# Performance work log

Hardware: AMD Instinct MI355X
Metric: run time of the kernel (lower is better)

## Reference

```python
import jax, jax.numpy as jnp
import numpy as np

N_NODES = 100000
N_EDGES = 1600000
NFEAT, NHID, NCLASS = 512, 256, 128
K_HOPS = 5
ALPHA = 0.1


def setup_inputs() -> dict:
    key = jax.random.key(0)
    ks = jax.random.split(key, 7)
    x = jax.random.normal(ks[0], (N_NODES, NFEAT), dtype=jnp.float32)
    edge_index = jax.random.randint(ks[1], (2, N_EDGES), 0, N_NODES, dtype=jnp.int64)
    edge_weight = jax.random.uniform(ks[2], (N_EDGES,), dtype=jnp.float32)
    # Glorot-ish scaled linear weights
    W1 = jax.random.normal(ks[3], (NFEAT, NHID), dtype=jnp.float32) * (1.0 / np.sqrt(NFEAT))
    b1 = jnp.zeros((NHID,), dtype=jnp.float32)
    W2 = jax.random.normal(ks[4], (NHID, NCLASS), dtype=jnp.float32) * (1.0 / np.sqrt(NHID))
    b2 = jnp.zeros((NCLASS,), dtype=jnp.float32)
    return {"x": x, "edge_index": edge_index, "edge_weight": edge_weight,
            "W1": W1, "b1": b1, "W2": W2, "b2": b2}


def reference(x, edge_index, edge_weight, W1, b1, W2, b2):
    # 2-layer MLP (act after first layer only; dropout p=0)
    h = jnp.maximum(x @ W1 + b1, 0.0)
    h = h @ W2 + b2  # [N, nclass]
    src = edge_index[0]
    dst = edge_index[1]
    x0 = h

    def step(carry, _):
        # gather by source, scale by edge weight, scatter-add at target
        msg = carry[src] * edge_weight[:, None]          # [E, nclass]
        agg = jax.ops.segment_sum(msg, dst, num_segments=N_NODES)
        out = (1.0 - ALPHA) * agg + ALPHA * x0           # restart mix
        return out, None

    xK, _ = jax.lax.scan(step, x0, None, length=K_HOPS)
    return jax.nn.log_softmax(xK, axis=1)
```

## Files before the change

### kernel.cpp

```cpp
#include <hip/hip_runtime.h>
#include <hip/hip_bf16.h>
#include <cstdint>
#include <cstddef>

#define N_NODES 100000
#define NFEAT 512
#define NHID 256
#define NCLASS 128
#define K_HOPS 5
#define ALPHA 0.1f

typedef __attribute__((ext_vector_type(8))) short short8v;
typedef __attribute__((ext_vector_type(4))) float f32x4;

__device__ __forceinline__ unsigned short f2bf(float f) {
    unsigned u = __builtin_bit_cast(unsigned, f);
    u += 0x7FFFu + ((u >> 16) & 1u);
    return (unsigned short)(u >> 16);
}
__device__ __forceinline__ float bflo(unsigned u) {
    return __builtin_bit_cast(float, u << 16);
}
__device__ __forceinline__ float bfhi(unsigned u) {
    return __builtin_bit_cast(float, u & 0xFFFF0000u);
}


__global__ void count_kernel(const int* __restrict__ dst, int* __restrict__ counts, int E) {
    int i = blockIdx.x * blockDim.x + threadIdx.x;
    if (i < E) atomicAdd(&counts[dst[i]], 1);
}

__global__ __launch_bounds__(256) void scan_p1(const int* __restrict__ counts,
                                               int* __restrict__ partial, int n) {
    __shared__ int ws[4];
    int b = blockIdx.x, t = threadIdx.x;
    int base = b * 1024 + t * 4;
    int s = 0;
#pragma unroll
    for (int j = 0; j < 4; ++j) {
        int idx = base + j;
        if (idx < n) s += counts[idx];
    }
#pragma unroll
    for (int off = 32; off; off >>= 1) s += __shfl_xor(s, off, 64);
    if ((t & 63) == 0) ws[t >> 6] = s;
    __syncthreads();
    if (t == 0) partial[b] = ws[0] + ws[1] + ws[2] + ws[3];
}

__global__ __launch_bounds__(128) void scan_p2(int* __restrict__ partial, int nb) {
    __shared__ int s[128];
    int t = threadIdx.x;
    int v = (t < nb) ? partial[t] : 0;
    s[t] = v;
    __syncthreads();
    for (int off = 1; off < 128; off <<= 1) {
        int u = (t >= off) ? s[t - off] : 0;
        __syncthreads();
        s[t] += u;
        __syncthreads();
    }
    if (t < nb) partial[t] = (t == 0) ? 0 : s[t - 1];
}

__global__ __launch_bounds__(256) void scan_p3(const int* __restrict__ counts,
                                               const int* __restrict__ partial,
                                               int* __restrict__ row_ptr,
                                               int* __restrict__ fill, int n) {
    __shared__ int ts[256];
    int b = blockIdx.x, t = threadIdx.x;
    int base = b * 1024 + t * 4;
    int c[4];
#pragma unroll
    for (int j = 0; j < 4; ++j) {
        int idx = base + j;
        c[j] = (idx < n) ? counts[idx] : 0;
    }
    int s = c[0] + c[1] + c[2] + c[3];
    ts[t] = s;
    __syncthreads();
    for (int off = 1; off < 256; off <<= 1) {
        int v = (t >= off) ? ts[t - off] : 0;
        __syncthreads();
        ts[t] += v;
        __syncthreads();
    }
    int pre = partial[b] + ((t == 0) ? 0 : ts[t - 1]);
#pragma unroll
    for (int j = 0; j < 4; ++j) {
        int idx = base + j;
        if (idx < n) {
            row_ptr[idx] = pre;
            fill[idx] = pre;
            if (idx == n - 1) row_ptr[n] = pre + c[j];
            pre += c[j];
        }
    }
}

__global__ void scatter_kernel(const int* __restrict__ src, const int* __restrict__ dst,
                               const float* __restrict__ w, int* __restrict__ fill,
                               int* __restrict__ col, float* __restrict__ wsorted, int E) {
    int i = blockIdx.x * blockDim.x + threadIdx.x;
    if (i < E) {
        int d = dst[i];
        int pos = atomicAdd(&fill[d], 1);
        col[pos] = src[i];
        wsorted[pos] = w[i];
    }
}

__global__ void wtrans_kernel(const float* __restrict__ W, unsigned short* __restrict__ Wt,
                              int K, int N) {
    int idx = blockIdx.x * blockDim.x + threadIdx.x;
    if (idx >= N * K) return;
    int n = idx / K, k = idx - n * K;
    Wt[idx] = f2bf(W[(size_t)k * N + n]);
}


__global__ __launch_bounds__(256) void gemm1_mfma(const float* __restrict__ X,
                                                  const unsigned short* __restrict__ W1t,
                                                  const float* __restrict__ b1,
                                                  unsigned short* __restrict__ Hb, int M) {
    __shared__ unsigned short As[128 * 32];
    __shared__ unsigned short Bs[128 * 32];
    const int tid = threadIdx.x;
    const int lane = tid & 63;
    const int wv = tid >> 6;
    const int wr = wv >> 1, wc = wv & 1;
    const int brow = blockIdx.y * 128;
    const int bcol = blockIdx.x * 128;

    f32x4 acc[4][4];
#pragma unroll
    for (int m = 0; m < 4; ++m)
#pragma unroll
        for (int n = 0; n < 4; ++n) acc[m][n] = f32x4{0.f, 0.f, 0.f, 0.f};

    for (int k0 = 0; k0 < NFEAT; k0 += 32) {
#pragma unroll
        for (int cc = 0; cc < 2; ++cc) {
            int c = tid + cc * 256;
            int m = c >> 2, kg = (c & 3) << 3;
            int row = brow + m; if (row > M - 1) row = M - 1;
            const float4 v0 = *(const float4*)&X[(size_t)row * NFEAT + k0 + kg];
            const float4 v1 = *(const float4*)&X[(size_t)row * NFEAT + k0 + kg + 4];
            short8v pk;
            pk[0] = (short)f2bf(v0.x); pk[1] = (short)f2bf(v0.y);
            pk[2] = (short)f2bf(v0.z); pk[3] = (short)f2bf(v0.w);
            pk[4] = (short)f2bf(v1.x); pk[5] = (short)f2bf(v1.y);
            pk[6] = (short)f2bf(v1.z); pk[7] = (short)f2bf(v1.w);
            *(short8v*)&As[c * 8] = pk;
        }
#pragma unroll
        for (int cc = 0; cc < 2; ++cc) {
            int c = tid + cc * 256;
            int n = c >> 2, kg = (c & 3) << 3;
            *(short8v*)&Bs[c * 8] = *(const short8v*)&W1t[(size_t)(bcol + n) * NFEAT + k0 + kg];
        }
        __syncthreads();
        short8v a[4], b[4];
#pragma unroll
        for (int m = 0; m < 4; ++m)
            a[m] = *(const short8v*)&As[((wr * 64 + m * 16 + (lane & 15)) * 4 + (lane >> 4)) * 8];
#pragma unroll
        for (int n = 0; n < 4; ++n)
            b[n] = *(const short8v*)&Bs[((wc * 64 + n * 16 + (lane & 15)) * 4 + (lane >> 4)) * 8];
#pragma unroll
        for (int m = 0; m < 4; ++m)
#pragma unroll
            for (int n = 0; n < 4; ++n)
                acc[m][n] = __builtin_amdgcn_mfma_f32_16x16x32_bf16(a[m], b[n], acc[m][n], 0, 0, 0);
        __syncthreads();
    }

#pragma unroll
    for (int n = 0; n < 4; ++n) {
        int colg = bcol + wc * 64 + n * 16 + (lane & 15);
        float bias = b1[colg];
#pragma unroll
        for (int m = 0; m < 4; ++m) {
#pragma unroll
            for (int r = 0; r < 4; ++r) {
                int rowg = brow + wr * 64 + m * 16 + (lane >> 4) * 4 + r;
                if (rowg < M) {
                    float vl = fmaxf(acc[m][n][r] + bias, 0.f);
                    Hb[(size_t)rowg * NHID + colg] = f2bf(vl);
                }
            }
        }
    }
}

__global__ __launch_bounds__(256) void gemm2_mfma(const unsigned short* __restrict__ Hb,
                                                  const unsigned short* __restrict__ W2t,
                                                  const float* __restrict__ b2,
                                                  unsigned short* __restrict__ C0, int M) {
    __shared__ unsigned short As[128 * 32];
    __shared__ unsigned short Bs[128 * 32];
    const int tid = threadIdx.x;
    const int lane = tid & 63;
    const int wv = tid >> 6;
    const int wr = wv >> 1, wc = wv & 1;
    const int brow = blockIdx.y * 128;

    f32x4 acc[4][4];
#pragma unroll
    for (int m = 0; m < 4; ++m)
#pragma unroll
        for (int n = 0; n < 4; ++n) acc[m][n] = f32x4{0.f, 0.f, 0.f, 0.f};

    for (int k0 = 0; k0 < NHID; k0 += 32) {
#pragma unroll
        for (int cc = 0; cc < 2; ++cc) {
            int c = tid + cc * 256;
            int m = c >> 2, kg = (c & 3) << 3;
            int row = brow + m; if (row > M - 1) row = M - 1;
            *(short8v*)&As[c * 8] = *(const short8v*)&Hb[(size_t)row * NHID + k0 + kg];
        }
#pragma unroll
        for (int cc = 0; cc < 2; ++cc) {
            int c = tid + cc * 256;
            int n = c >> 2, kg = (c & 3) << 3;
            *(short8v*)&Bs[c * 8] = *(const short8v*)&W2t[(size_t)n * NHID + k0 + kg];
        }
        __syncthreads();
        short8v a[4], b[4];
#pragma unroll
        for (int m = 0; m < 4; ++m)
            a[m] = *(const short8v*)&As[((wr * 64 + m * 16 + (lane & 15)) * 4 + (lane >> 4)) * 8];
#pragma unroll
        for (int n = 0; n < 4; ++n)
            b[n] = *(const short8v*)&Bs[((wc * 64 + n * 16 + (lane & 15)) * 4 + (lane >> 4)) * 8];
#pragma unroll
        for (int m = 0; m < 4; ++m)
#pragma unroll
            for (int n = 0; n < 4; ++n)
                acc[m][n] = __builtin_amdgcn_mfma_f32_16x16x32_bf16(a[m], b[n], acc[m][n], 0, 0, 0);
        __syncthreads();
    }

#pragma unroll
    for (int n = 0; n < 4; ++n) {
        int colg = wc * 64 + n * 16 + (lane & 15);
        float bias = b2[colg];
#pragma unroll
        for (int m = 0; m < 4; ++m) {
#pragma unroll
            for (int r = 0; r < 4; ++r) {
                int rowg = brow + wr * 64 + m * 16 + (lane >> 4) * 4 + r;
                if (rowg < M)
                    C0[(size_t)rowg * NCLASS + colg] = f2bf(acc[m][n][r] + bias);
            }
        }
    }
}

template<int FINAL>
__global__ __launch_bounds__(256) void hop_kernel(const unsigned short* __restrict__ carry,
                                                  const unsigned short* __restrict__ c0,
                                                  const int* __restrict__ rp,
                                                  const int* __restrict__ col,
                                                  const float* __restrict__ ew,
                                                  unsigned short* __restrict__ outb,
                                                  float* __restrict__ outf, int nnodes) {
    int node = blockIdx.x * 4 + (threadIdx.x >> 6);
    if (node >= nnodes) return;
    int lane = threadIdx.x & 63;
    int e0 = rp[node], e1 = rp[node + 1];

    float a0x = 0.f, a0y = 0.f, a1x = 0.f, a1y = 0.f;
    float a2x = 0.f, a2y = 0.f, a3x = 0.f, a3y = 0.f;

    for (int eb = e0; eb < e1; eb += 64) {
        int nb = e1 - eb; if (nb > 64) nb = 64;
        int cs = 0, wvi = 0;
        if (lane < nb) {
            cs = col[eb + lane];
            wvi = __builtin_bit_cast(int, ew[eb + lane]);
        }
        int j = 0;
        for (; j + 3 < nb; j += 4) {
            int s0 = __builtin_amdgcn_readlane(cs, j);
            int s1 = __builtin_amdgcn_readlane(cs, j + 1);
            int s2 = __builtin_amdgcn_readlane(cs, j + 2);
            int s3 = __builtin_amdgcn_readlane(cs, j + 3);
            float w0 = __builtin_bit_cast(float, __builtin_amdgcn_readlane(wvi, j));
            float w1 = __builtin_bit_cast(float, __builtin_amdgcn_readlane(wvi, j + 1));
            float w2 = __builtin_bit_cast(float, __builtin_amdgcn_readlane(wvi, j + 2));
            float w3 = __builtin_bit_cast(float, __builtin_amdgcn_readlane(wvi, j + 3));
            unsigned u0 = ((const unsigned*)(carry + ((size_t)s0 << 7)))[lane];
            unsigned u1 = ((const unsigned*)(carry + ((size_t)s1 << 7)))[lane];
            unsigned u2 = ((const unsigned*)(carry + ((size_t)s2 << 7)))[lane];
            unsigned u3 = ((const unsigned*)(carry + ((size_t)s3 << 7)))[lane];
            a0x = fmaf(w0, bflo(u0), a0x); a0y = fmaf(w0, bfhi(u0), a0y);
            a1x = fmaf(w1, bflo(u1), a1x); a1y = fmaf(w1, bfhi(u1), a1y);
            a2x = fmaf(w2, bflo(u2), a2x); a2y = fmaf(w2, bfhi(u2), a2y);
            a3x = fmaf(w3, bflo(u3), a3x); a3y = fmaf(w3, bfhi(u3), a3y);
        }
        for (; j < nb; ++j) {
            int s0 = __builtin_amdgcn_readlane(cs, j);
            float w0 = __builtin_bit_cast(float, __builtin_amdgcn_readlane(wvi, j));
            unsigned u0 = ((const unsigned*)(carry + ((size_t)s0 << 7)))[lane];
            a0x = fmaf(w0, bflo(u0), a0x); a0y = fmaf(w0, bfhi(u0), a0y);
        }
    }

    unsigned ux = ((const unsigned*)(c0 + ((size_t)node << 7)))[lane];
    float vx = (1.f - ALPHA) * (a0x + a1x + a2x + a3x) + ALPHA * bflo(ux);
    float vy = (1.f - ALPHA) * (a0y + a1y + a2y + a3y) + ALPHA * bfhi(ux);

    if (FINAL) {
        float mx = fmaxf(vx, vy);
#pragma unroll
        for (int off = 32; off; off >>= 1) mx = fmaxf(mx, __shfl_xor(mx, off, 64));
        float se = __expf(vx - mx) + __expf(vy - mx);
#pragma unroll
        for (int off = 32; off; off >>= 1) se += __shfl_xor(se, off, 64);
        float l = mx + __logf(se);
        float2 o; o.x = vx - l; o.y = vy - l;
        ((float2*)(outf + ((size_t)node << 7)))[lane] = o;
    } else {
        unsigned o = (unsigned)f2bf(vx) | ((unsigned)f2bf(vy) << 16);
        ((unsigned*)(outb + ((size_t)node << 7)))[lane] = o;
    }
}


extern "C" void kernel_launch(void* const* d_in, const int* in_sizes, int n_in,
                              void* d_out, int out_size, void* d_ws, size_t ws_size,
                              hipStream_t stream) {
    const float* x   = (const float*)d_in[0];
    const int*   ei  = (const int*)d_in[1];
    const float* ew  = (const float*)d_in[2];
    const float* W1  = (const float*)d_in[3];
    const float* b1  = (const float*)d_in[4];
    const float* W2  = (const float*)d_in[5];
    const float* b2  = (const float*)d_in[6];
    float* outp = (float*)d_out;

    const int E = in_sizes[1] / 2;
    const int Nn = N_NODES;
    const int* srcv = ei;
    const int* dstv = ei + E;
    const size_t NC = (size_t)Nn * NCLASS;

    unsigned short* c0  = (unsigned short*)d_ws;
    unsigned short* A16 = c0 + NC;
    unsigned short* B16 = A16 + NC;
    unsigned short* hb  = A16;
    unsigned short* w1t = B16 + NC;
    unsigned short* w2t = w1t + NHID * NFEAT;
    int* row_ptr = (int*)(w2t + NCLASS * NHID);
    int* fill    = row_ptr + (Nn + 1);
    int* partial = fill + Nn;
    int* col     = partial + 128;
    float* wsorted = (float*)(col + E);

    const int NB = (Nn + 1023) / 1024;

    hipMemsetAsync(fill, 0, (size_t)Nn * sizeof(int), stream);
    count_kernel<<<(E + 255) / 256, 256, 0, stream>>>(dstv, fill, E);
    scan_p1<<<NB, 256, 0, stream>>>(fill, partial, Nn);
    scan_p2<<<1, 128, 0, stream>>>(partial, NB);
    scan_p3<<<NB, 256, 0, stream>>>(fill, partial, row_ptr, fill, Nn);
    scatter_kernel<<<(E + 255) / 256, 256, 0, stream>>>(srcv, dstv, ew, fill, col, wsorted, E);

    wtrans_kernel<<<(NHID * NFEAT + 255) / 256, 256, 0, stream>>>(W1, w1t, NFEAT, NHID);
    wtrans_kernel<<<(NCLASS * NHID + 255) / 256, 256, 0, stream>>>(W2, w2t, NHID, NCLASS);

    {
        dim3 g1(NHID / 128, (Nn + 127) / 128);
        gemm1_mfma<<<g1, 256, 0, stream>>>(x, w1t, b1, hb, Nn);
        dim3 g2(1, (Nn + 127) / 128);
        gemm2_mfma<<<g2, 256, 0, stream>>>(hb, w2t, b2, c0, Nn);
    }

    int grid = (Nn + 3) / 4;
    const unsigned short* carry = c0;
    unsigned short* dsts[2] = {A16, B16};
    for (int k = 0; k < K_HOPS - 1; ++k) {
        unsigned short* o = dsts[k & 1];
        hop_kernel<0><<<grid, 256, 0, stream>>>(carry, c0, row_ptr, col, wsorted, o, nullptr, Nn);
        carry = o;
    }
    hop_kernel<1><<<grid, 256, 0, stream>>>(carry, c0, row_ptr, col, wsorted, nullptr, outp, Nn);
}
```

Before: 664.9 us.

## Prefetch GEMM tiles into registers, pack edge arrays, unroll hop gather by eight

```diff
diff --git a/kernel.cpp b/kernel.cpp
--- a/kernel.cpp
+++ b/kernel.cpp
@@ -23,6 +23,11 @@
 }
 __device__ __forceinline__ float bfhi(unsigned u) {
     return __builtin_bit_cast(float, u & 0xFFFF0000u);
+}
+__device__ __forceinline__ unsigned cvtpk2(float a, float b) {
+    unsigned r;
+    asm("v_cvt_pk_bf16_f32 %0, %1, %2" : "=v"(r) : "v"(a), "v"(b));
+    return r;
 }
 
 
@@ -101,13 +106,13 @@
 
 __global__ void scatter_kernel(const int* __restrict__ src, const int* __restrict__ dst,
                                const float* __restrict__ w, int* __restrict__ fill,
-                               int* __restrict__ col, float* __restrict__ wsorted, int E) {
+                               int2* __restrict__ epk, int E) {
     int i = blockIdx.x * blockDim.x + threadIdx.x;
     if (i < E) {
         int d = dst[i];
         int pos = atomicAdd(&fill[d], 1);
-        col[pos] = src[i];
-        wsorted[pos] = w[i];
+        int2 m; m.x = src[i]; m.y = __builtin_bit_cast(int, w[i]);
+        epk[pos] = m;
     }
 }
 
@@ -119,19 +124,32 @@
     Wt[idx] = f2bf(W[(size_t)k * N + n]);
 }
 
-
-__global__ __launch_bounds__(256) void gemm1_mfma(const float* __restrict__ X,
-                                                  const unsigned short* __restrict__ W1t,
-                                                  const float* __restrict__ b1,
-                                                  unsigned short* __restrict__ Hb, int M) {
-    __shared__ unsigned short As[128 * 32];
-    __shared__ unsigned short Bs[128 * 32];
+template<int K, int N, int RELU, int AF32>
+__global__ __launch_bounds__(256) void gemm_mfma(const void* __restrict__ Ain,
+                                                 const unsigned short* __restrict__ Wt,
+                                                 const float* __restrict__ bias,
+                                                 unsigned short* __restrict__ Cout, int M) {
+    __shared__ unsigned short As[4096];
+    __shared__ unsigned short Bs[4096];
     const int tid = threadIdx.x;
     const int lane = tid & 63;
     const int wv = tid >> 6;
     const int wr = wv >> 1, wc = wv & 1;
     const int brow = blockIdx.y * 128;
     const int bcol = blockIdx.x * 128;
+    const float* Af = (const float*)Ain;
+    const unsigned short* Ab = (const unsigned short*)Ain;
+
+    int arow[2], browb[2], kc[2];
+#pragma unroll
+    for (int i = 0; i < 2; ++i) {
+        int g = tid + i * 256, l6 = g & 63;
+        int r = (g >> 6) * 16 + (l6 & 15);
+        kc[i] = (l6 >> 4) * 8;
+        int ra = brow + r; if (ra > M - 1) ra = M - 1;
+        arow[i] = ra;
+        browb[i] = bcol + r;
+    }
 
     f32x4 acc[4][4];
 #pragma unroll
@@ -139,35 +157,59 @@
 #pragma unroll
         for (int n = 0; n < 4; ++n) acc[m][n] = f32x4{0.f, 0.f, 0.f, 0.f};
 
-    for (int k0 = 0; k0 < NFEAT; k0 += 32) {
-#pragma unroll
-        for (int cc = 0; cc < 2; ++cc) {
-            int c = tid + cc * 256;
-            int m = c >> 2, kg = (c & 3) << 3;
-            int row = brow + m; if (row > M - 1) row = M - 1;
-            const float4 v0 = *(const float4*)&X[(size_t)row * NFEAT + k0 + kg];
-            const float4 v1 = *(const float4*)&X[(size_t)row * NFEAT + k0 + kg + 4];
-            short8v pk;
-            pk[0] = (short)f2bf(v0.x); pk[1] = (short)f2bf(v0.y);
-            pk[2] = (short)f2bf(v0.z); pk[3] = (short)f2bf(v0.w);
-            pk[4] = (short)f2bf(v1.x); pk[5] = (short)f2bf(v1.y);
-            pk[6] = (short)f2bf(v1.z); pk[7] = (short)f2bf(v1.w);
-            *(short8v*)&As[c * 8] = pk;
-        }
-#pragma unroll
-        for (int cc = 0; cc < 2; ++cc) {
-            int c = tid + cc * 256;
-            int n = c >> 2, kg = (c & 3) << 3;
-            *(short8v*)&Bs[c * 8] = *(const short8v*)&W1t[(size_t)(bcol + n) * NFEAT + k0 + kg];
-        }
-        __syncthreads();
+    float4 pa0[2], pa1[2];
+    short8v pab[2];
+    short8v pb[2];
+
+#pragma unroll
+    for (int i = 0; i < 2; ++i) {
+        if constexpr (AF32) {
+            const float* s = &Af[(size_t)arow[i] * K + kc[i]];
+            pa0[i] = *(const float4*)s;
+            pa1[i] = *(const float4*)(s + 4);
+        } else {
+            pab[i] = *(const short8v*)&Ab[(size_t)arow[i] * K + kc[i]];
+        }
+        pb[i] = *(const short8v*)&Wt[(size_t)browb[i] * K + kc[i]];
+    }
+
+    for (int k0 = 0; k0 < K; k0 += 32) {
+#pragma unroll
+        for (int i = 0; i < 2; ++i) {
+            int g = tid + i * 256;
+            if constexpr (AF32) {
+                uint4 u;
+                u.x = cvtpk2(pa0[i].x, pa0[i].y);
+                u.y = cvtpk2(pa0[i].z, pa0[i].w);
+                u.z = cvtpk2(pa1[i].x, pa1[i].y);
+                u.w = cvtpk2(pa1[i].z, pa1[i].w);
+                *(uint4*)&As[g * 8] = u;
+            } else {
+                *(short8v*)&As[g * 8] = pab[i];
+            }
+            *(short8v*)&Bs[g * 8] = pb[i];
+        }
+        __syncthreads();
+        if (k0 + 32 < K) {
+#pragma unroll
+            for (int i = 0; i < 2; ++i) {
+                if constexpr (AF32) {
+                    const float* s = &Af[(size_t)arow[i] * K + k0 + 32 + kc[i]];
+                    pa0[i] = *(const float4*)s;
+                    pa1[i] = *(const float4*)(s + 4);
+                } else {
+                    pab[i] = *(const short8v*)&Ab[(size_t)arow[i] * K + k0 + 32 + kc[i]];
+                }
+                pb[i] = *(const short8v*)&Wt[(size_t)browb[i] * K + k0 + 32 + kc[i]];
+            }
+        }
         short8v a[4], b[4];
 #pragma unroll
         for (int m = 0; m < 4; ++m)
-            a[m] = *(const short8v*)&As[((wr * 64 + m * 16 + (lane & 15)) * 4 + (lane >> 4)) * 8];
+            a[m] = *(const short8v*)&As[((wr * 4 + m) * 64 + lane) * 8];
 #pragma unroll
         for (int n = 0; n < 4; ++n)
-            b[n] = *(const short8v*)&Bs[((wc * 64 + n * 16 + (lane & 15)) * 4 + (lane >> 4)) * 8];
+            b[n] = *(const short8v*)&Bs[((wc * 4 + n) * 64 + lane) * 8];
 #pragma unroll
         for (int m = 0; m < 4; ++m)
 #pragma unroll
@@ -179,80 +221,17 @@
 #pragma unroll
     for (int n = 0; n < 4; ++n) {
         int colg = bcol + wc * 64 + n * 16 + (lane & 15);
-        float bias = b1[colg];
+        float bv = bias[colg];
 #pragma unroll
         for (int m = 0; m < 4; ++m) {
 #pragma unroll
             for (int r = 0; r < 4; ++r) {
                 int rowg = brow + wr * 64 + m * 16 + (lane >> 4) * 4 + r;
                 if (rowg < M) {
-                    float vl = fmaxf(acc[m][n][r] + bias, 0.f);
-                    Hb[(size_t)rowg * NHID + colg] = f2bf(vl);
+                    float v = acc[m][n][r] + bv;
+                    if constexpr (RELU) v = fmaxf(v, 0.f);
+                    Cout[(size_t)rowg * N + colg] = f2bf(v);
                 }
-            }
-        }
-    }
-}
-
-__global__ __launch_bounds__(256) void gemm2_mfma(const unsigned short* __restrict__ Hb,
-                                                  const unsigned short* __restrict__ W2t,
-                                                  const float* __restrict__ b2,
-                                                  unsigned short* __restrict__ C0, int M) {
-    __shared__ unsigned short As[128 * 32];
-    __shared__ unsigned short Bs[128 * 32];
-    const int tid = threadIdx.x;
-    const int lane = tid & 63;
-    const int wv = tid >> 6;
-    const int wr = wv >> 1, wc = wv & 1;
-    const int brow = blockIdx.y * 128;
-
-    f32x4 acc[4][4];
-#pragma unroll
-    for (int m = 0; m < 4; ++m)
-#pragma unroll
-        for (int n = 0; n < 4; ++n) acc[m][n] = f32x4{0.f, 0.f, 0.f, 0.f};
-
-    for (int k0 = 0; k0 < NHID; k0 += 32) {
-#pragma unroll
-        for (int cc = 0; cc < 2; ++cc) {
-            int c = tid + cc * 256;
-            int m = c >> 2, kg = (c & 3) << 3;
-            int row = brow + m; if (row > M - 1) row = M - 1;
-            *(short8v*)&As[c * 8] = *(const short8v*)&Hb[(size_t)row * NHID + k0 + kg];
-        }
-#pragma unroll
-        for (int cc = 0; cc < 2; ++cc) {
-            int c = tid + cc * 256;
-            int n = c >> 2, kg = (c & 3) << 3;
-            *(short8v*)&Bs[c * 8] = *(const short8v*)&W2t[(size_t)n * NHID + k0 + kg];
-        }
-        __syncthreads();
-        short8v a[4], b[4];
-#pragma unroll
-        for (int m = 0; m < 4; ++m)
-            a[m] = *(const short8v*)&As[((wr * 64 + m * 16 + (lane & 15)) * 4 + (lane >> 4)) * 8];
-#pragma unroll
-        for (int n = 0; n < 4; ++n)
-            b[n] = *(const short8v*)&Bs[((wc * 64 + n * 16 + (lane & 15)) * 4 + (lane >> 4)) * 8];
-#pragma unroll
-        for (int m = 0; m < 4; ++m)
-#pragma unroll
-            for (int n = 0; n < 4; ++n)
-                acc[m][n] = __builtin_amdgcn_mfma_f32_16x16x32_bf16(a[m], b[n], acc[m][n], 0, 0, 0);
-        __syncthreads();
-    }
-
-#pragma unroll
-    for (int n = 0; n < 4; ++n) {
-        int colg = wc * 64 + n * 16 + (lane & 15);
-        float bias = b2[colg];
-#pragma unroll
-        for (int m = 0; m < 4; ++m) {
-#pragma unroll
-            for (int r = 0; r < 4; ++r) {
-                int rowg = brow + wr * 64 + m * 16 + (lane >> 4) * 4 + r;
-                if (rowg < M)
-                    C0[(size_t)rowg * NCLASS + colg] = f2bf(acc[m][n][r] + bias);
             }
         }
     }
@@ -262,8 +241,7 @@
 __global__ __launch_bounds__(256) void hop_kernel(const unsigned short* __restrict__ carry,
                                                   const unsigned short* __restrict__ c0,
                                                   const int* __restrict__ rp,
-                                                  const int* __restrict__ col,
-                                                  const float* __restrict__ ew,
+                                                  const int2* __restrict__ epk,
                                                   unsigned short* __restrict__ outb,
                                                   float* __restrict__ outf, int nnodes) {
     int node = blockIdx.x * 4 + (threadIdx.x >> 6);
@@ -278,10 +256,44 @@
         int nb = e1 - eb; if (nb > 64) nb = 64;
         int cs = 0, wvi = 0;
         if (lane < nb) {
-            cs = col[eb + lane];
-            wvi = __builtin_bit_cast(int, ew[eb + lane]);
+            int2 m = epk[eb + lane];
+            cs = m.x; wvi = m.y;
         }
         int j = 0;
+        for (; j + 7 < nb; j += 8) {
+            int s0 = __builtin_amdgcn_readlane(cs, j);
+            int s1 = __builtin_amdgcn_readlane(cs, j + 1);
+            int s2 = __builtin_amdgcn_readlane(cs, j + 2);
+            int s3 = __builtin_amdgcn_readlane(cs, j + 3);
+            int s4 = __builtin_amdgcn_readlane(cs, j + 4);
+            int s5 = __builtin_amdgcn_readlane(cs, j + 5);
+            int s6 = __builtin_amdgcn_readlane(cs, j + 6);
+            int s7 = __builtin_amdgcn_readlane(cs, j + 7);
+            float w0 = __builtin_bit_cast(float, __builtin_amdgcn_readlane(wvi, j));
+            float w1 = __builtin_bit_cast(float, __builtin_amdgcn_readlane(wvi, j + 1));
+            float w2 = __builtin_bit_cast(float, __builtin_amdgcn_readlane(wvi, j + 2));
+            float w3 = __builtin_bit_cast(float, __builtin_amdgcn_readlane(wvi, j + 3));
+            float w4 = __builtin_bit_cast(float, __builtin_amdgcn_readlane(wvi, j + 4));
+            float w5 = __builtin_bit_cast(float, __builtin_amdgcn_readlane(wvi, j + 5));
+            float w6 = __builtin_bit_cast(float, __builtin_amdgcn_readlane(wvi, j + 6));
+            float w7 = __builtin_bit_cast(float, __builtin_amdgcn_readlane(wvi, j + 7));
+            unsigned u0 = ((const unsigned*)(carry + ((size_t)s0 << 7)))[lane];
+            unsigned u1 = ((const unsigned*)(carry + ((size_t)s1 << 7)))[lane];
+            unsigned u2 = ((const unsigned*)(carry + ((size_t)s2 << 7)))[lane];
+            unsigned u3 = ((const unsigned*)(carry + ((size_t)s3 << 7)))[lane];
+            unsigned u4 = ((const unsigned*)(carry + ((size_t)s4 << 7)))[lane];
+            unsigned u5 = ((const unsigned*)(carry + ((size_t)s5 << 7)))[lane];
+            unsigned u6 = ((const unsigned*)(carry + ((size_t)s6 << 7)))[lane];
+            unsigned u7 = ((const unsigned*)(carry + ((size_t)s7 << 7)))[lane];
+            a0x = fmaf(w0, bflo(u0), a0x); a0y = fmaf(w0, bfhi(u0), a0y);
+            a1x = fmaf(w1, bflo(u1), a1x); a1y = fmaf(w1, bfhi(u1), a1y);
+            a2x = fmaf(w2, bflo(u2), a2x); a2y = fmaf(w2, bfhi(u2), a2y);
+            a3x = fmaf(w3, bflo(u3), a3x); a3y = fmaf(w3, bfhi(u3), a3y);
+            a0x = fmaf(w4, bflo(u4), a0x); a0y = fmaf(w4, bfhi(u4), a0y);
+            a1x = fmaf(w5, bflo(u5), a1x); a1y = fmaf(w5, bfhi(u5), a1y);
+            a2x = fmaf(w6, bflo(u6), a2x); a2y = fmaf(w6, bfhi(u6), a2y);
+            a3x = fmaf(w7, bflo(u7), a3x); a3y = fmaf(w7, bfhi(u7), a3y);
+        }
         for (; j + 3 < nb; j += 4) {
             int s0 = __builtin_amdgcn_readlane(cs, j);
             int s1 = __builtin_amdgcn_readlane(cs, j + 1);
@@ -356,8 +368,7 @@
     int* row_ptr = (int*)(w2t + NCLASS * NHID);
     int* fill    = row_ptr + (Nn + 1);
     int* partial = fill + Nn;
-    int* col     = partial + 128;
-    float* wsorted = (float*)(col + E);
+    int2* epk    = (int2*)(partial + 128);
 
     const int NB = (Nn + 1023) / 1024;
 
@@ -366,16 +377,16 @@
     scan_p1<<<NB, 256, 0, stream>>>(fill, partial, Nn);
     scan_p2<<<1, 128, 0, stream>>>(partial, NB);
     scan_p3<<<NB, 256, 0, stream>>>(fill, partial, row_ptr, fill, Nn);
-    scatter_kernel<<<(E + 255) / 256, 256, 0, stream>>>(srcv, dstv, ew, fill, col, wsorted, E);
+    scatter_kernel<<<(E + 255) / 256, 256, 0, stream>>>(srcv, dstv, ew, fill, epk, E);
 
     wtrans_kernel<<<(NHID * NFEAT + 255) / 256, 256, 0, stream>>>(W1, w1t, NFEAT, NHID);
     wtrans_kernel<<<(NCLASS * NHID + 255) / 256, 256, 0, stream>>>(W2, w2t, NHID, NCLASS);
 
     {
         dim3 g1(NHID / 128, (Nn + 127) / 128);
-        gemm1_mfma<<<g1, 256, 0, stream>>>(x, w1t, b1, hb, Nn);
-        dim3 g2(1, (Nn + 127) / 128);
-        gemm2_mfma<<<g2, 256, 0, stream>>>(hb, w2t, b2, c0, Nn);
+        gemm_mfma<NFEAT, NHID, 1, 1><<<g1, 256, 0, stream>>>(x, w1t, b1, hb, Nn);
+        dim3 g2(NCLASS / 128, (Nn + 127) / 128);
+        gemm_mfma<NHID, NCLASS, 0, 0><<<g2, 256, 0, stream>>>(hb, w2t, b2, c0, Nn);
     }
 
     int grid = (Nn + 3) / 4;
@@ -383,8 +394,8 @@
     unsigned short* dsts[2] = {A16, B16};
     for (int k = 0; k < K_HOPS - 1; ++k) {
         unsigned short* o = dsts[k & 1];
-        hop_kernel<0><<<grid, 256, 0, stream>>>(carry, c0, row_ptr, col, wsorted, o, nullptr, Nn);
+        hop_kernel<0><<<grid, 256, 0, stream>>>(carry, c0, row_ptr, epk, o, nullptr, Nn);
         carry = o;
     }
-    hop_kernel<1><<<grid, 256, 0, stream>>>(carry, c0, row_ptr, col, wsorted, nullptr, outp, Nn);
-}
+    hop_kernel<1><<<grid, 256, 0, stream>>>(carry, c0, row_ptr, epk, nullptr, outp, Nn);
+}
```

Result: slower. 684.6 us (+3.0%).
